# Optimization experiments

Hardware: AMD Instinct MI355X
Metric: run time of the kernel (lower is better)

## Reference

```python
import jax, jax.numpy as jnp
import numpy as np

N_NODES = 65536   # N
D_HID   = 128     # D (hidden)
N_GROUPS = 16384  # G portfolios
GROUP_LEN = 64    # lines per portfolio (port_len entries)
N_LINES = N_GROUPS * GROUP_LEN  # L
BATCH = 16384     # B samples


def setup_inputs() -> dict:
    key = jax.random.key(0)
    k = jax.random.split(key, 5)
    H = jax.random.normal(k[0], (N_NODES, D_HID), dtype=jnp.float32)
    port_w_signed_flat = jax.random.normal(k[1], (N_LINES,), dtype=jnp.float32)
    anchor_idx = jax.random.randint(k[2], (BATCH,), 0, N_NODES, dtype=jnp.int32)
    pf_gid = jax.random.randint(k[3], (BATCH,), 0, N_GROUPS, dtype=jnp.int32)
    port_nodes_flat = jax.random.randint(k[4], (N_LINES,), 0, N_NODES, dtype=jnp.int32)
    port_len = jnp.full((N_GROUPS,), GROUP_LEN, dtype=jnp.int32)
    return {
        'H': H,
        'port_w_signed_flat': port_w_signed_flat,
        'anchor_idx': anchor_idx,
        'pf_gid': pf_gid,
        'port_nodes_flat': port_nodes_flat,
        'port_len': port_len,
    }


def reference(H, port_w_signed_flat, anchor_idx, pf_gid, port_nodes_flat, port_len):
    """Faithful, vectorized port of compute_samplewise_portfolio_vectors_loo.

    Ragged segment-weighted mean per portfolio group, with strict leave-one-out
    correction for each sample's anchor node, followed by L2 normalization.
    Returns (V_abs, V_sgn), each [B, D].
    """
    N, D = H.shape
    G = port_len.shape[0]
    L = port_nodes_flat.shape[0]

    # gid per flat line: repeat_interleave(arange(G), lens)
    gid_lines = jnp.repeat(jnp.arange(G, dtype=jnp.int32), port_len,
                           total_repeat_length=L)

    w_abs = jnp.abs(port_w_signed_flat)
    Hl = H[port_nodes_flat]                                  # [L, D] gather
    S_abs = jax.ops.segment_sum(w_abs[:, None] * Hl, gid_lines, num_segments=G)
    W_abs = jax.ops.segment_sum(w_abs, gid_lines, num_segments=G)
    W_sgn = jax.ops.segment_sum(port_w_signed_flat, gid_lines, num_segments=G)

    valid = (pf_gid >= 0) & (pf_gid < G)
    g = jnp.clip(pf_gid, 0, G - 1)

    # Leave-one-out self-weight: sum of w over lines where (gid==g_i, node==anchor_i).
    # Vectorized join via a sorted composite int32 key (G*N < 2^31 by construction).
    keys_l = gid_lines * N + port_nodes_flat                 # [L]
    keys_s = g * N + anchor_idx                              # [B]
    order = jnp.argsort(keys_l)
    sk = keys_l[order]
    zero1 = jnp.zeros((1,), H.dtype)
    ca = jnp.concatenate([zero1, jnp.cumsum(w_abs[order])])
    cs = jnp.concatenate([zero1, jnp.cumsum(port_w_signed_flat[order])])
    lo = jnp.searchsorted(sk, keys_s, side='left')
    hi = jnp.searchsorted(sk, keys_s, side='right')
    self_w_abs = ca[hi] - ca[lo]                             # [B]
    self_w_sgn = cs[hi] - cs[lo]                             # [B]

    Ha = H[anchor_idx]                                       # [B, D]
    denom = jnp.maximum(W_abs[g] - self_w_abs, 1e-12)        # clamp_min
    V_abs = (S_abs[g] - self_w_abs[:, None] * Ha) / denom[:, None]
    V_sgn = ((W_sgn[g] - self_w_sgn) / denom)[:, None] * V_abs

    V_abs = jnp.where(valid[:, None], V_abs, jnp.zeros((), H.dtype))
    V_sgn = jnp.where(valid[:, None], V_sgn, jnp.zeros((), H.dtype))

    # torch F.normalize: x / clamp(||x||, min=eps)
    na = jnp.linalg.norm(V_abs, axis=1, keepdims=True)
    V_abs = V_abs / jnp.maximum(na, 1e-6)
    ns = jnp.linalg.norm(V_sgn, axis=1, keepdims=True)
    V_sgn = jnp.where(ns > 0, V_sgn / jnp.maximum(ns, 1e-6), V_sgn)
    return V_abs, V_sgn
```

## Files before the change

### kernel.cpp

```cpp
#include <hip/hip_runtime.h>
#include <hip/hip_bf16.h>


__global__ __launch_bounds__(1024) void scan_offsets_kernel(
    const int* __restrict__ len, int* __restrict__ offs, int G) {
    __shared__ int part[1024];
    const int t = threadIdx.x;
    const int chunk = (G + 1023) >> 10;
    const int lo = min(t * chunk, G);
    const int hi = min(lo + chunk, G);
    int s = 0;
    for (int i = lo; i < hi; ++i) s += len[i];
    part[t] = s;
    __syncthreads();
    #pragma unroll
    for (int ofs = 1; ofs < 1024; ofs <<= 1) {
        int v = (t >= ofs) ? part[t - ofs] : 0;
        __syncthreads();
        part[t] += v;
        __syncthreads();
    }
    int run = part[t] - s;
    for (int i = lo; i < hi; ++i) { offs[i] = run; run += len[i]; }
}

__device__ inline unsigned bf_rne(float x) {
    unsigned u = __float_as_uint(x);
    return (u + 0x7FFFu + ((u >> 16) & 1u)) >> 16;
}

__global__ __launch_bounds__(256) void convert_h_kernel(
    const float4* __restrict__ H4, uint2* __restrict__ Hb, int n4) {
    const int i = blockIdx.x * blockDim.x + threadIdx.x;
    if (i >= n4) return;
    const float4 v = H4[i];
    uint2 o;
    o.x = bf_rne(v.x) | (bf_rne(v.y) << 16);
    o.y = bf_rne(v.z) | (bf_rne(v.w) << 16);
    Hb[i] = o;
}

__device__ inline void unpack2(unsigned d, float& lo, float& hi) {
    lo = __uint_as_float(d << 16);
    hi = __uint_as_float(d & 0xFFFF0000u);
}

__global__ __launch_bounds__(256) void pf_loo_bf16(
    const unsigned short* __restrict__ Hb,
    const float* __restrict__ pw,
    const int* __restrict__ anchor_idx,
    const int* __restrict__ pf_gid,
    const int* __restrict__ pn,
    const int* __restrict__ plen,
    const int* __restrict__ offs,
    float* __restrict__ out, int B, int G) {
    const int b = blockIdx.x * (blockDim.x >> 6) + (threadIdx.x >> 6);
    const int lane = threadIdx.x & 63;
    const int q = lane >> 4;
    const int s = lane & 15;
    if (b >= B) return;

    float4* outA = (float4*)(out + (size_t)b * 128);
    float4* outS = (float4*)(out + ((size_t)B + b) * 128);

    const int gid = pf_gid[b];
    if (!(gid >= 0 && gid < G)) {
        const float4 z = make_float4(0.f, 0.f, 0.f, 0.f);
        if (q == 0) { outA[2 * s] = z; outA[2 * s + 1] = z; }
        if (q == 1) { outS[2 * s] = z; outS[2 * s + 1] = z; }
        return;
    }

    const int anchor = anchor_idx[b];
    const int off = offs[gid];
    const int len = plen[gid];

    float acc[8] = {0.f, 0.f, 0.f, 0.f, 0.f, 0.f, 0.f, 0.f};
    float laWa = 0.f, laWs = 0.f, laSa = 0.f, laSs = 0.f;

    for (int base = 0; base < len; base += 64) {
        const int jmax = min(64, len - base);
        float wl = 0.f;
        int nl = 0;
        if (lane < jmax) {
            wl = pw[off + base + lane];
            nl = pn[off + base + lane];
        }
        const float wla = fabsf(wl);
        laWa += wla;
        laWs += wl;
        if (nl == anchor) { laSa += wla; laSs += wl; }

        #pragma unroll 8
        for (int jj = 0; jj < 64; jj += 4) {
            const float ww = fabsf(__shfl(wl, jj + q));
            const int row = __shfl(nl, jj + q);
            const uint4 h = *((const uint4*)(Hb + (size_t)row * 128) + s);
            float f0, f1, f2, f3, f4, f5, f6, f7;
            unpack2(h.x, f0, f1);
            unpack2(h.y, f2, f3);
            unpack2(h.z, f4, f5);
            unpack2(h.w, f6, f7);
            acc[0] = fmaf(ww, f0, acc[0]);
            acc[1] = fmaf(ww, f1, acc[1]);
            acc[2] = fmaf(ww, f2, acc[2]);
            acc[3] = fmaf(ww, f3, acc[3]);
            acc[4] = fmaf(ww, f4, acc[4]);
            acc[5] = fmaf(ww, f5, acc[5]);
            acc[6] = fmaf(ww, f6, acc[6]);
            acc[7] = fmaf(ww, f7, acc[7]);
        }
    }

    #pragma unroll
    for (int m = 32; m; m >>= 1) {
        laWa += __shfl_xor(laWa, m);
        laWs += __shfl_xor(laWs, m);
        laSa += __shfl_xor(laSa, m);
        laSs += __shfl_xor(laSs, m);
    }
    #pragma unroll
    for (int k = 0; k < 8; ++k) {
        acc[k] += __shfl_xor(acc[k], 16);
        acc[k] += __shfl_xor(acc[k], 32);
    }

    const float denom = fmaxf(laWa - laSa, 1e-12f);
    const uint4 ha = *((const uint4*)(Hb + (size_t)anchor * 128) + s);
    float h0, h1, h2, h3, h4, h5, h6, h7;
    unpack2(ha.x, h0, h1);
    unpack2(ha.y, h2, h3);
    unpack2(ha.z, h4, h5);
    unpack2(ha.w, h6, h7);
    const float hv[8] = {h0, h1, h2, h3, h4, h5, h6, h7};

    float v[8];
    float n2 = 0.f;
    #pragma unroll
    for (int k = 0; k < 8; ++k) {
        v[k] = (acc[k] - laSa * hv[k]) / denom;
        n2 = fmaf(v[k], v[k], n2);
    }
    const float scale = (laWs - laSs) / denom;

    #pragma unroll
    for (int m = 32; m; m >>= 1) n2 += __shfl_xor(n2, m);
    n2 *= 0.25f;
    const float na = sqrtf(n2);

    const float invA = 1.0f / fmaxf(na, 1e-6f);
    const float ns = fabsf(scale) * na;
    const float sgnscale = (ns > 0.f) ? (scale / fmaxf(ns, 1e-6f)) : scale;

    if (q == 0) {
        outA[2 * s] = make_float4(v[0] * invA, v[1] * invA, v[2] * invA, v[3] * invA);
        outA[2 * s + 1] = make_float4(v[4] * invA, v[5] * invA, v[6] * invA, v[7] * invA);
    } else if (q == 1) {
        outS[2 * s] = make_float4(v[0] * sgnscale, v[1] * sgnscale, v[2] * sgnscale, v[3] * sgnscale);
        outS[2 * s + 1] = make_float4(v[4] * sgnscale, v[5] * sgnscale, v[6] * sgnscale, v[7] * sgnscale);
    }
}

__global__ __launch_bounds__(256) void pf_loo_f32(
    const float* __restrict__ H, const float* __restrict__ pw,
    const int* __restrict__ anchor_idx, const int* __restrict__ pf_gid,
    const int* __restrict__ pn, const int* __restrict__ plen,
    const int* __restrict__ offs, float* __restrict__ out, int B, int G) {
    const int b = blockIdx.x * (blockDim.x >> 6) + (threadIdx.x >> 6);
    const int lane = threadIdx.x & 63;
    const int half = lane >> 5;
    const int qlane = lane & 31;
    if (b >= B) return;
    float4* outA = (float4*)(out + (size_t)b * 128);
    float4* outS = (float4*)(out + ((size_t)B + b) * 128);
    const int gid = pf_gid[b];
    if (!(gid >= 0 && gid < G)) {
        float4 z = make_float4(0.f, 0.f, 0.f, 0.f);
        if (half == 0) { outA[qlane] = z; outS[qlane] = z; }
        return;
    }
    const int anchor = anchor_idx[b];
    const int off = offs[gid];
    const int len = plen[gid];
    float4 acc = make_float4(0.f, 0.f, 0.f, 0.f);
    float laWa = 0.f, laWs = 0.f, laSa = 0.f, laSs = 0.f;
    for (int base = 0; base < len; base += 64) {
        const int jmax = min(64, len - base);
        float wl = 0.f;
        int nl = 0;
        if (lane < jmax) { wl = pw[off + base + lane]; nl = pn[off + base + lane]; }
        const float wla = fabsf(wl);
        laWa += wla; laWs += wl;
        if (nl == anchor) { laSa += wla; laSs += wl; }
        #pragma unroll 8
        for (int jj = 0; jj < 64; jj += 2) {
            const float ww = fabsf(__shfl(wl, jj + half));
            const int row = __shfl(nl, jj + half);
            const float4 h = ((const float4*)(H + (size_t)row * 128))[qlane];
            acc.x = fmaf(ww, h.x, acc.x);
            acc.y = fmaf(ww, h.y, acc.y);
            acc.z = fmaf(ww, h.z, acc.z);
            acc.w = fmaf(ww, h.w, acc.w);
        }
    }
    #pragma unroll
    for (int m = 32; m; m >>= 1) {
        laWa += __shfl_xor(laWa, m);
        laWs += __shfl_xor(laWs, m);
        laSa += __shfl_xor(laSa, m);
        laSs += __shfl_xor(laSs, m);
    }
    acc.x += __shfl_xor(acc.x, 32);
    acc.y += __shfl_xor(acc.y, 32);
    acc.z += __shfl_xor(acc.z, 32);
    acc.w += __shfl_xor(acc.w, 32);
    const float denom = fmaxf(laWa - laSa, 1e-12f);
    const float4 hv = ((const float4*)(H + (size_t)anchor * 128))[qlane];
    float4 v;
    v.x = (acc.x - laSa * hv.x) / denom;
    v.y = (acc.y - laSa * hv.y) / denom;
    v.z = (acc.z - laSa * hv.z) / denom;
    v.w = (acc.w - laSa * hv.w) / denom;
    const float scale = (laWs - laSs) / denom;
    float n2 = v.x * v.x + v.y * v.y + v.z * v.z + v.w * v.w;
    #pragma unroll
    for (int m = 32; m; m >>= 1) n2 += __shfl_xor(n2, m);
    n2 *= 0.5f;
    const float na = sqrtf(n2);
    const float invA = 1.0f / fmaxf(na, 1e-6f);
    const float ns = fabsf(scale) * na;
    const float sgnscale = (ns > 0.f) ? (scale / fmaxf(ns, 1e-6f)) : scale;
    const float sc = half ? sgnscale : invA;
    float4 res = make_float4(v.x * sc, v.y * sc, v.z * sc, v.w * sc);
    float4* dst = half ? outS : outA;
    dst[qlane] = res;
}

extern "C" void kernel_launch(void* const* d_in, const int* in_sizes, int n_in,
                              void* d_out, int out_size, void* d_ws, size_t ws_size,
                              hipStream_t stream) {
    const float* H      = (const float*)d_in[0];
    const float* pw     = (const float*)d_in[1];
    const int* anchor   = (const int*)d_in[2];
    const int* gid      = (const int*)d_in[3];
    const int* pn       = (const int*)d_in[4];
    const int* plen     = (const int*)d_in[5];
    float* out          = (float*)d_out;

    const int B = in_sizes[2];
    const int G = in_sizes[5];
    const int ND = in_sizes[0];
    const size_t hb_bytes = (size_t)ND * 2;

    const int wavesPerBlock = 4;
    const int blocks = (B + wavesPerBlock - 1) / wavesPerBlock;

    if (ws_size >= hb_bytes + (size_t)G * 4) {
        unsigned short* Hb = (unsigned short*)d_ws;
        int* offsp = (int*)((char*)d_ws + hb_bytes);
        const int n4 = ND / 4;
        convert_h_kernel<<<(n4 + 255) / 256, 256, 0, stream>>>(
            (const float4*)H, (uint2*)Hb, n4);
        scan_offsets_kernel<<<1, 1024, 0, stream>>>(plen, offsp, G);
        pf_loo_bf16<<<blocks, 256, 0, stream>>>(Hb, pw, anchor, gid, pn, plen,
                                                offsp, out, B, G);
    } else {
        int* offsp = (int*)d_ws;
        scan_offsets_kernel<<<1, 1024, 0, stream>>>(plen, offsp, G);
        pf_loo_f32<<<blocks, 256, 0, stream>>>(H, pw, anchor, gid, pn, plen,
                                               offsp, out, B, G);
    }
}
```

Before: 147.3 us.

## Compute per-group weighted sums once, then apply leave-one-out per sample

```diff
diff --git a/kernel.cpp b/kernel.cpp
--- a/kernel.cpp
+++ b/kernel.cpp
@@ -2,15 +2,50 @@
 #include <hip/hip_bf16.h>
 
 
-__global__ __launch_bounds__(1024) void scan_offsets_kernel(
-    const int* __restrict__ len, int* __restrict__ offs, int G) {
+#define DDIM 128
+
+__device__ inline unsigned bf_rne(float x) {
+    unsigned u = __float_as_uint(x);
+    return (u + 0x7FFFu + ((u >> 16) & 1u)) >> 16;
+}
+
+__device__ inline void unpack2(unsigned d, float& lo, float& hi) {
+    lo = __uint_as_float(d << 16);
+    hi = __uint_as_float(d & 0xFFFF0000u);
+}
+
+__global__ __launch_bounds__(1024) void init_kernel(
+    const float4* __restrict__ H4, uint2* __restrict__ Hb, int n4,
+    const int* __restrict__ plen, int* __restrict__ offs, int G,
+    const int* __restrict__ pf_gid, int* __restrict__ used, int B, int nconv) {
+    const int t = threadIdx.x;
+    const int bb = blockIdx.x;
+    if (bb < nconv) {
+        const int i = bb * 1024 + t;
+        if (i < n4) {
+            const float4 v = H4[i];
+            uint2 o;
+            o.x = bf_rne(v.x) | (bf_rne(v.y) << 16);
+            o.y = bf_rne(v.z) | (bf_rne(v.w) << 16);
+            Hb[i] = o;
+        }
+        return;
+    }
+    if (bb == nconv) {
+        for (int i = t; i < G; i += 1024) used[i] = 0;
+        __syncthreads();
+        for (int i = t; i < B; i += 1024) {
+            const int g = pf_gid[i];
+            if (g >= 0 && g < G) used[g] = 1;
+        }
+        return;
+    }
     __shared__ int part[1024];
-    const int t = threadIdx.x;
     const int chunk = (G + 1023) >> 10;
     const int lo = min(t * chunk, G);
     const int hi = min(lo + chunk, G);
     int s = 0;
-    for (int i = lo; i < hi; ++i) s += len[i];
+    for (int i = lo; i < hi; ++i) s += plen[i];
     part[t] = s;
     __syncthreads();
     #pragma unroll
@@ -21,62 +56,27 @@
         __syncthreads();
     }
     int run = part[t] - s;
-    for (int i = lo; i < hi; ++i) { offs[i] = run; run += len[i]; }
-}
-
-__device__ inline unsigned bf_rne(float x) {
-    unsigned u = __float_as_uint(x);
-    return (u + 0x7FFFu + ((u >> 16) & 1u)) >> 16;
-}
-
-__global__ __launch_bounds__(256) void convert_h_kernel(
-    const float4* __restrict__ H4, uint2* __restrict__ Hb, int n4) {
-    const int i = blockIdx.x * blockDim.x + threadIdx.x;
-    if (i >= n4) return;
-    const float4 v = H4[i];
-    uint2 o;
-    o.x = bf_rne(v.x) | (bf_rne(v.y) << 16);
-    o.y = bf_rne(v.z) | (bf_rne(v.w) << 16);
-    Hb[i] = o;
-}
-
-__device__ inline void unpack2(unsigned d, float& lo, float& hi) {
-    lo = __uint_as_float(d << 16);
-    hi = __uint_as_float(d & 0xFFFF0000u);
-}
-
-__global__ __launch_bounds__(256) void pf_loo_bf16(
+    for (int i = lo; i < hi; ++i) { offs[i] = run; run += plen[i]; }
+}
+
+__global__ __launch_bounds__(256) void group_sums(
     const unsigned short* __restrict__ Hb,
-    const float* __restrict__ pw,
-    const int* __restrict__ anchor_idx,
-    const int* __restrict__ pf_gid,
-    const int* __restrict__ pn,
-    const int* __restrict__ plen,
-    const int* __restrict__ offs,
-    float* __restrict__ out, int B, int G) {
-    const int b = blockIdx.x * (blockDim.x >> 6) + (threadIdx.x >> 6);
+    const float* __restrict__ pw, const int* __restrict__ pn,
+    const int* __restrict__ plen, const int* __restrict__ offs,
+    const int* __restrict__ used,
+    float* __restrict__ Sabs, float* __restrict__ Wag,
+    float* __restrict__ Wsg, int G) {
+    const int g = blockIdx.x * (blockDim.x >> 6) + (threadIdx.x >> 6);
     const int lane = threadIdx.x & 63;
     const int q = lane >> 4;
     const int s = lane & 15;
-    if (b >= B) return;
-
-    float4* outA = (float4*)(out + (size_t)b * 128);
-    float4* outS = (float4*)(out + ((size_t)B + b) * 128);
-
-    const int gid = pf_gid[b];
-    if (!(gid >= 0 && gid < G)) {
-        const float4 z = make_float4(0.f, 0.f, 0.f, 0.f);
-        if (q == 0) { outA[2 * s] = z; outA[2 * s + 1] = z; }
-        if (q == 1) { outS[2 * s] = z; outS[2 * s + 1] = z; }
-        return;
-    }
-
-    const int anchor = anchor_idx[b];
-    const int off = offs[gid];
-    const int len = plen[gid];
+    if (g >= G || !used[g]) return;
+
+    const int off = offs[g];
+    const int len = plen[g];
 
     float acc[8] = {0.f, 0.f, 0.f, 0.f, 0.f, 0.f, 0.f, 0.f};
-    float laWa = 0.f, laWs = 0.f, laSa = 0.f, laSs = 0.f;
+    float laWa = 0.f, laWs = 0.f;
 
     for (int base = 0; base < len; base += 64) {
         const int jmax = min(64, len - base);
@@ -86,16 +86,14 @@
             wl = pw[off + base + lane];
             nl = pn[off + base + lane];
         }
-        const float wla = fabsf(wl);
-        laWa += wla;
+        laWa += fabsf(wl);
         laWs += wl;
-        if (nl == anchor) { laSa += wla; laSs += wl; }
 
         #pragma unroll 8
         for (int jj = 0; jj < 64; jj += 4) {
             const float ww = fabsf(__shfl(wl, jj + q));
             const int row = __shfl(nl, jj + q);
-            const uint4 h = *((const uint4*)(Hb + (size_t)row * 128) + s);
+            const uint4 h = *((const uint4*)(Hb + (size_t)row * DDIM) + s);
             float f0, f1, f2, f3, f4, f5, f6, f7;
             unpack2(h.x, f0, f1);
             unpack2(h.y, f2, f3);
@@ -116,8 +114,6 @@
     for (int m = 32; m; m >>= 1) {
         laWa += __shfl_xor(laWa, m);
         laWs += __shfl_xor(laWs, m);
-        laSa += __shfl_xor(laSa, m);
-        laSs += __shfl_xor(laSs, m);
     }
     #pragma unroll
     for (int k = 0; k < 8; ++k) {
@@ -125,40 +121,102 @@
         acc[k] += __shfl_xor(acc[k], 32);
     }
 
-    const float denom = fmaxf(laWa - laSa, 1e-12f);
-    const uint4 ha = *((const uint4*)(Hb + (size_t)anchor * 128) + s);
-    float h0, h1, h2, h3, h4, h5, h6, h7;
-    unpack2(ha.x, h0, h1);
-    unpack2(ha.y, h2, h3);
-    unpack2(ha.z, h4, h5);
-    unpack2(ha.w, h6, h7);
-    const float hv[8] = {h0, h1, h2, h3, h4, h5, h6, h7};
-
-    float v[8];
-    float n2 = 0.f;
-    #pragma unroll
-    for (int k = 0; k < 8; ++k) {
-        v[k] = (acc[k] - laSa * hv[k]) / denom;
-        n2 = fmaf(v[k], v[k], n2);
-    }
-    const float scale = (laWs - laSs) / denom;
-
+    if (q == 0) {
+        float4* dst = (float4*)(Sabs + (size_t)g * DDIM);
+        dst[2 * s] = make_float4(acc[0], acc[1], acc[2], acc[3]);
+        dst[2 * s + 1] = make_float4(acc[4], acc[5], acc[6], acc[7]);
+    }
+    if (lane == 0) { Wag[g] = laWa; Wsg[g] = laWs; }
+}
+
+__global__ __launch_bounds__(256) void per_sample(
+    const unsigned short* __restrict__ Hb,
+    const float* __restrict__ pw, const int* __restrict__ pn,
+    const int* __restrict__ plen, const int* __restrict__ offs,
+    const float* __restrict__ Sabs, const float* __restrict__ Wag,
+    const float* __restrict__ Wsg,
+    const int* __restrict__ anchor_idx, const int* __restrict__ pf_gid,
+    float* __restrict__ out, int B, int G) {
+    const int b = blockIdx.x * (blockDim.x >> 6) + (threadIdx.x >> 6);
+    const int lane = threadIdx.x & 63;
+    if (b >= B) return;
+
+    float2* outA = (float2*)(out + (size_t)b * DDIM);
+    float2* outS = (float2*)(out + ((size_t)B + b) * DDIM);
+
+    const int g = pf_gid[b];
+    if (!(g >= 0 && g < G)) {
+        const float2 z = make_float2(0.f, 0.f);
+        outA[lane] = z;
+        outS[lane] = z;
+        return;
+    }
+
+    const int anchor = anchor_idx[b];
+    const int off = offs[g];
+    const int len = plen[g];
+
+    float selfa = 0.f, selfs = 0.f;
+    for (int base = 0; base < len; base += 64) {
+        const int jmax = min(64, len - base);
+        if (lane < jmax) {
+            const float w = pw[off + base + lane];
+            const int n = pn[off + base + lane];
+            if (n == anchor) { selfa += fabsf(w); selfs += w; }
+        }
+    }
+    #pragma unroll
+    for (int m = 32; m; m >>= 1) {
+        selfa += __shfl_xor(selfa, m);
+        selfs += __shfl_xor(selfs, m);
+    }
+
+    const float Wa = Wag[g];
+    const float Wsn = Wsg[g];
+    const float2 S = ((const float2*)(Sabs + (size_t)g * DDIM))[lane];
+    const unsigned hb = *((const unsigned*)(Hb + (size_t)anchor * DDIM) + lane);
+    float h0, h1;
+    unpack2(hb, h0, h1);
+
+    const float denom = fmaxf(Wa - selfa, 1e-12f);
+    float2 v;
+    v.x = (S.x - selfa * h0) / denom;
+    v.y = (S.y - selfa * h1) / denom;
+    const float scale = (Wsn - selfs) / denom;
+
+    float n2 = v.x * v.x + v.y * v.y;
     #pragma unroll
     for (int m = 32; m; m >>= 1) n2 += __shfl_xor(n2, m);
-    n2 *= 0.25f;
     const float na = sqrtf(n2);
 
     const float invA = 1.0f / fmaxf(na, 1e-6f);
     const float ns = fabsf(scale) * na;
     const float sgnscale = (ns > 0.f) ? (scale / fmaxf(ns, 1e-6f)) : scale;
 
-    if (q == 0) {
-        outA[2 * s] = make_float4(v[0] * invA, v[1] * invA, v[2] * invA, v[3] * invA);
-        outA[2 * s + 1] = make_float4(v[4] * invA, v[5] * invA, v[6] * invA, v[7] * invA);
-    } else if (q == 1) {
-        outS[2 * s] = make_float4(v[0] * sgnscale, v[1] * sgnscale, v[2] * sgnscale, v[3] * sgnscale);
-        outS[2 * s + 1] = make_float4(v[4] * sgnscale, v[5] * sgnscale, v[6] * sgnscale, v[7] * sgnscale);
-    }
+    outA[lane] = make_float2(v.x * invA, v.y * invA);
+    outS[lane] = make_float2(v.x * sgnscale, v.y * sgnscale);
+}
+
+__global__ __launch_bounds__(1024) void scan_only(
+    const int* __restrict__ len, int* __restrict__ offs, int G) {
+    __shared__ int part[1024];
+    const int t = threadIdx.x;
+    const int chunk = (G + 1023) >> 10;
+    const int lo = min(t * chunk, G);
+    const int hi = min(lo + chunk, G);
+    int s = 0;
+    for (int i = lo; i < hi; ++i) s += len[i];
+    part[t] = s;
+    __syncthreads();
+    #pragma unroll
+    for (int ofs = 1; ofs < 1024; ofs <<= 1) {
+        int v = (t >= ofs) ? part[t - ofs] : 0;
+        __syncthreads();
+        part[t] += v;
+        __syncthreads();
+    }
+    int run = part[t] - s;
+    for (int i = lo; i < hi; ++i) { offs[i] = run; run += len[i]; }
 }
 
 __global__ __launch_bounds__(256) void pf_loo_f32(
@@ -171,8 +229,8 @@
     const int half = lane >> 5;
     const int qlane = lane & 31;
     if (b >= B) return;
-    float4* outA = (float4*)(out + (size_t)b * 128);
-    float4* outS = (float4*)(out + ((size_t)B + b) * 128);
+    float4* outA = (float4*)(out + (size_t)b * DDIM);
+    float4* outS = (float4*)(out + ((size_t)B + b) * DDIM);
     const int gid = pf_gid[b];
     if (!(gid >= 0 && gid < G)) {
         float4 z = make_float4(0.f, 0.f, 0.f, 0.f);
@@ -196,7 +254,7 @@
         for (int jj = 0; jj < 64; jj += 2) {
             const float ww = fabsf(__shfl(wl, jj + half));
             const int row = __shfl(nl, jj + half);
-            const float4 h = ((const float4*)(H + (size_t)row * 128))[qlane];
+            const float4 h = ((const float4*)(H + (size_t)row * DDIM))[qlane];
             acc.x = fmaf(ww, h.x, acc.x);
             acc.y = fmaf(ww, h.y, acc.y);
             acc.z = fmaf(ww, h.z, acc.z);
@@ -215,7 +273,7 @@
     acc.z += __shfl_xor(acc.z, 32);
     acc.w += __shfl_xor(acc.w, 32);
     const float denom = fmaxf(laWa - laSa, 1e-12f);
-    const float4 hv = ((const float4*)(H + (size_t)anchor * 128))[qlane];
+    const float4 hv = ((const float4*)(H + (size_t)anchor * DDIM))[qlane];
     float4 v;
     v.x = (acc.x - laSa * hv.x) / denom;
     v.y = (acc.y - laSa * hv.y) / denom;
@@ -251,22 +309,34 @@
     const int G = in_sizes[5];
     const int ND = in_sizes[0];
     const size_t hb_bytes = (size_t)ND * 2;
-
-    const int wavesPerBlock = 4;
-    const int blocks = (B + wavesPerBlock - 1) / wavesPerBlock;
-
-    if (ws_size >= hb_bytes + (size_t)G * 4) {
-        unsigned short* Hb = (unsigned short*)d_ws;
-        int* offsp = (int*)((char*)d_ws + hb_bytes);
+    const size_t sabs_bytes = (size_t)G * DDIM * 4;
+    const size_t need = hb_bytes + sabs_bytes + (size_t)G * 4 * 4;
+
+    if (ws_size >= need) {
+        char* p = (char*)d_ws;
+        unsigned short* Hb = (unsigned short*)p;        p += hb_bytes;
+        float* Sabs        = (float*)p;                 p += sabs_bytes;
+        int* offsp         = (int*)p;                   p += (size_t)G * 4;
+        int* usedp         = (int*)p;                   p += (size_t)G * 4;
+        float* Wag         = (float*)p;                 p += (size_t)G * 4;
+        float* Wsg         = (float*)p;
+
         const int n4 = ND / 4;
-        convert_h_kernel<<<(n4 + 255) / 256, 256, 0, stream>>>(
-            (const float4*)H, (uint2*)Hb, n4);
-        scan_offsets_kernel<<<1, 1024, 0, stream>>>(plen, offsp, G);
-        pf_loo_bf16<<<blocks, 256, 0, stream>>>(Hb, pw, anchor, gid, pn, plen,
-                                                offsp, out, B, G);
+        const int nconv = (n4 + 1023) / 1024;
+        init_kernel<<<nconv + 2, 1024, 0, stream>>>(
+            (const float4*)H, (uint2*)Hb, n4, plen, offsp, G, gid, usedp, B, nconv);
+
+        const int gblocks = (G + 3) / 4;
+        group_sums<<<gblocks, 256, 0, stream>>>(Hb, pw, pn, plen, offsp, usedp,
+                                                Sabs, Wag, Wsg, G);
+
+        const int sblocks = (B + 3) / 4;
+        per_sample<<<sblocks, 256, 0, stream>>>(Hb, pw, pn, plen, offsp, Sabs,
+                                                Wag, Wsg, anchor, gid, out, B, G);
     } else {
         int* offsp = (int*)d_ws;
-        scan_offsets_kernel<<<1, 1024, 0, stream>>>(plen, offsp, G);
+        scan_only<<<1, 1024, 0, stream>>>(plen, offsp, G);
+        const int blocks = (B + 3) / 4;
         pf_loo_f32<<<blocks, 256, 0, stream>>>(H, pw, anchor, gid, pn, plen,
                                                offsp, out, B, G);
     }
```

After: 142.6 us. -3.2%, faster.
